# Kernel optimization log

Measured on AMD Instinct MI355X. Metric: run time of the kernel, lower is better.

## Reference

```python
import jax, jax.numpy as jnp
import numpy as np

N_QUBITS = 12
N_LAYERS = 4
BATCH = 1024


def _ry(theta):
    # Batched RY(theta): (...,) -> (..., 2, 2) complex64
    c = jnp.cos(theta / 2)
    s = jnp.sin(theta / 2)
    m = jnp.stack([jnp.stack([c, -s], -1), jnp.stack([s, c], -1)], -2)
    return m.astype(jnp.complex64)


def _rot(phi, theta, omega):
    # PennyLane Rot(phi, theta, omega) = RZ(omega) @ RY(theta) @ RZ(phi)
    c = jnp.cos(theta / 2)
    s = jnp.sin(theta / 2)
    ep = jnp.exp(-0.5j * (phi + omega))  # e^{-i(phi+omega)/2}
    em = jnp.exp(0.5j * (phi - omega))   # e^{ i(phi-omega)/2}
    m00 = ep * c
    m01 = -em * s
    m10 = jnp.conj(em) * s
    m11 = jnp.conj(ep) * c
    m = jnp.stack([jnp.stack([m00, m01], -1), jnp.stack([m10, m11], -1)], -2)
    return m.astype(jnp.complex64)


def _apply_1q(state, U, wire, n):
    # state: (B, 2^n); U: (2,2) or batched (B,2,2). Wire 0 = most significant bit.
    B = state.shape[0]
    st = state.reshape(B, 2 ** wire, 2, 2 ** (n - 1 - wire))
    if U.ndim == 2:
        st = jnp.einsum('ij,bajc->baic', U, st)
    else:
        st = jnp.einsum('bij,bajc->baic', U, st)
    return st.reshape(B, 2 ** n)


def _cnot(state, c, t, n):
    # CNOT(control=c, target=t): flip target bit where control bit == 1.
    B = state.shape[0]
    lo, hi = (c, t) if c < t else (t, c)
    st = state.reshape(B, 2 ** lo, 2, 2 ** (hi - lo - 1), 2, 2 ** (n - 1 - hi))
    c_ax = 2 if c < t else 4
    t_ax = 6 - c_ax
    s0 = jax.lax.index_in_dim(st, 0, c_ax, keepdims=True)
    s1 = jax.lax.index_in_dim(st, 1, c_ax, keepdims=True)
    s1 = jnp.flip(s1, axis=t_ax)
    st = jnp.concatenate([s0, s1], axis=c_ax)
    return st.reshape(B, 2 ** n)


def _circuit(x, weights):
    # AngleEmbedding(rotation='Y') + StronglyEntanglingLayers + per-wire PauliZ expvals
    B, n = x.shape
    state = jnp.zeros((B, 2 ** n), jnp.complex64).at[:, 0].set(1.0)
    for w in range(n):  # angle embedding: RY(x[:, w]) on wire w (batched gate)
        state = _apply_1q(state, _ry(x[:, w]), w, n)
    n_layers = weights.shape[0]
    for l in range(n_layers):
        for w in range(n):
            state = _apply_1q(state, _rot(weights[l, w, 0], weights[l, w, 1], weights[l, w, 2]), w, n)
        r = (l % (n - 1)) + 1  # default StronglyEntanglingLayers range
        for w in range(n):
            state = _cnot(state, w, (w + r) % n, n)
    probs = jnp.real(state * jnp.conj(state))  # (B, 2^n)
    zs = []
    for w in range(n):
        p = probs.reshape(B, 2 ** w, 2, 2 ** (n - 1 - w))
        zs.append((p[:, :, 0, :] - p[:, :, 1, :]).sum((1, 2)))
    return jnp.stack(zs, -1)  # (B, n) PauliZ expectation values


def setup_inputs() -> dict:
    key = jax.random.key(0)
    k1, k2, k3 = jax.random.split(key, 3)
    x = jax.random.uniform(k1, (BATCH, N_QUBITS), jnp.float32, -jnp.pi, jnp.pi)
    weights = jax.random.uniform(k2, (N_LAYERS, N_QUBITS, 3), jnp.float32, 0.0, 2 * jnp.pi)
    head_w = jax.random.normal(k3, (1, N_QUBITS), jnp.float32) * 0.1
    head_b = jnp.zeros((1,), jnp.float32)
    return {"x": x, "weights": weights, "head_w": head_w, "head_b": head_b}


def reference(x, weights, head_w, head_b):
    z = _circuit(x, weights)              # (B, n_qubits), values in [-1, 1]
    y = z @ head_w.T + head_b             # (B, 1)
    return y[:, 0]                        # squeeze(-1)
```

## Files before the change

### kernel.cpp

```cpp
#include <hip/hip_runtime.h>

#define NQ 12
#define NSTATES 4096
#define NLAYERS 4
#define NGATES 48
#define NMERGED 12
#define NGROUPS 9
#define TPB 256

struct Sched { unsigned m[NGATES]; unsigned sel[NGATES]; unsigned zrow[NQ]; };

constexpr Sched make_sched() {
    Sched s{};
    unsigned rows[NQ] = {}, bcols[NQ] = {};
    for (int b = 0; b < NQ; ++b) { rows[b] = 1u << b; bcols[b] = 1u << b; }
    int g = 0;
    for (int w = 0; w < NQ; ++w) { int b = NQ - 1 - w; s.m[g] = bcols[b]; s.sel[g] = rows[b]; ++g; }
    for (int l = 0; l < NLAYERS; ++l) {
        if (l > 0)
            for (int w = 0; w < NQ; ++w) { int b = NQ - 1 - w; s.m[g] = bcols[b]; s.sel[g] = rows[b]; ++g; }
        int r = (l % (NQ - 1)) + 1;
        for (int w = 0; w < NQ; ++w) {
            int c = w, t = (w + r) % NQ;
            int bc = NQ - 1 - c, bt = NQ - 1 - t;
            rows[bt] ^= rows[bc];
            bcols[bc] ^= bcols[bt];
        }
    }
    for (int w = 0; w < NQ; ++w) s.zrow[w] = rows[NQ - 1 - w];
    return s;
}

constexpr unsigned swz(unsigned j) { return j ^ (((j >> 4) ^ (j >> 8)) & 0xFu); }

struct Group {
    unsigned sel[4];
    unsigned swzc[16];
    unsigned cparbits[4];
    int npos[8];
};
struct Plan {
    Group g[NGROUPS];
    unsigned zrow[NQ];
    unsigned zparbits[NQ];
};

constexpr bool inv4(const unsigned m[4], int p0, int p1, int p2, int p3) {
    int pv[4] = {p0, p1, p2, p3};
    unsigned rows[4] = {};
    for (int i = 0; i < 4; ++i) {
        unsigned r = 0;
        for (int k = 0; k < 4; ++k) r |= ((m[i] >> pv[k]) & 1u) << k;
        rows[i] = r;
    }
    unsigned used = 0; int rank = 0;
    for (int c = 0; c < 4; ++c) {
        int pr = -1;
        for (int r = 0; r < 4; ++r)
            if (!((used >> r) & 1u) && ((rows[r] >> c) & 1u)) { pr = r; break; }
        if (pr < 0) continue;
        used |= 1u << pr; ++rank;
        for (int r = 0; r < 4; ++r)
            if (r != pr && ((rows[r] >> c) & 1u)) rows[r] ^= rows[pr];
    }
    return rank == 4;
}

constexpr int popc12(unsigned v) { int c = 0; for (int i = 0; i < 12; ++i) c += (v >> i) & 1; return c; }
constexpr int msb12(unsigned v) { int m = -1; for (int i = 0; i < 12; ++i) if ((v >> i) & 1) m = i; return m; }

constexpr int coverage(const int piv[4]) {
    bool isp[12] = {};
    for (int i = 0; i < 4; ++i) isp[piv[i]] = true;
    bool seen[4] = {}; int cov = 0, cnt = 0;
    for (int p = 0; p < 12 && cnt < 6; ++p)
        if (!isp[p]) { if (!seen[p & 3]) { seen[p & 3] = true; ++cov; } ++cnt; }
    return cov;
}

constexpr Plan make_plan() {
    Sched s = make_sched();
    Plan pl{};
    for (int w = 0; w < NQ; ++w) pl.zrow[w] = s.zrow[w];
    for (int gi = 0; gi < NGROUPS; ++gi) {
        Group &G = pl.g[gi];
        unsigned m[4] = {};
        for (int i = 0; i < 4; ++i) {
            m[i] = s.m[NMERGED + gi * 4 + i];
            G.sel[i] = s.sel[NMERGED + gi * 4 + i];
        }
        int piv[4] = {};
        unsigned bas[4] = {};
        for (int i = 0; i < 4; ++i) {
            unsigned v = m[i];
            for (int k = 0; k < i; ++k) if ((v >> piv[k]) & 1u) v ^= bas[k];
            piv[i] = msb12(v);
            bas[i] = v;
        }
        if (coverage(piv) < 4) {
            int best[4] = {piv[0], piv[1], piv[2], piv[3]};
            int bestcov = coverage(piv);
            for (int a = 0; a < 4 && bestcov < 4; ++a) {
                for (int q = 0; q < 12 && bestcov < 4; ++q) {
                    bool dup = false;
                    for (int i = 0; i < 4; ++i) if (piv[i] == q) dup = true;
                    if (dup) continue;
                    int cand[4] = {piv[0], piv[1], piv[2], piv[3]};
                    cand[a] = q;
                    if (!inv4(m, cand[0], cand[1], cand[2], cand[3])) continue;
                    int cv = coverage(cand);
                    if (cv > bestcov) { bestcov = cv; for (int i = 0; i < 4; ++i) best[i] = cand[i]; }
                }
            }
            for (int i = 0; i < 4; ++i) piv[i] = best[i];
        }
        {
            bool isp[12] = {};
            for (int i = 0; i < 4; ++i) isp[piv[i]] = true;
            int k = 0;
            for (int p = 0; p < 12; ++p) if (!isp[p]) G.npos[k++] = p;
        }
        for (int e = 0; e < 16; ++e) {
            unsigned c = 0;
            for (int q = 0; q < 4; ++q) if ((e >> q) & 1) c ^= m[q];
            G.swzc[e] = swz(c);
        }
        for (int i = 0; i < 4; ++i) {
            unsigned bits = 0;
            for (int e = 0; e < 16; ++e) {
                unsigned c = 0;
                for (int q = 0; q < 4; ++q) if ((e >> q) & 1) c ^= m[q];
                if (popc12(c & G.sel[i]) & 1) bits |= 1u << e;
            }
            G.cparbits[i] = bits;
        }
        if (gi == NGROUPS - 1) {
            for (int w = 0; w < NQ; ++w) {
                unsigned bits = 0;
                for (int e = 0; e < 16; ++e) {
                    unsigned c = 0;
                    for (int q = 0; q < 4; ++q) if ((e >> q) & 1) c ^= m[q];
                    if (popc12(c & s.zrow[w]) & 1) bits |= 1u << e;
                }
                pl.zparbits[w] = bits;
            }
        }
    }
    return pl;
}

__device__ constexpr Plan PLAN = make_plan();

__device__ __forceinline__ float xorf(float a, unsigned s) {
    return __uint_as_float(__float_as_uint(a) ^ s);
}

template <int GI>
__device__ __forceinline__ void do_pass(int tid, float (&ar)[16], float (&ai)[16],
                                        unsigned &jr_out, float2* st, const float4* gmat)
{
    constexpr Group G = PLAN.g[GI];

    unsigned jr = 0;
    #pragma unroll
    for (int k = 0; k < 8; ++k) jr |= ((unsigned)(tid >> k) & 1u) << G.npos[k];
    const unsigned basev = jr ^ (((jr >> 4) ^ (jr >> 8)) & 0xFu);

    #pragma unroll
    for (int e = 0; e < 8; ++e) {
        float2 v = st[basev ^ G.swzc[e]];
        ar[e] = v.x; ai[e] = v.y;
    }

    {
        const float4 uv = gmat[NMERGED + GI * 4 + 0];
        const unsigned sgP = (unsigned)(__popc(jr & G.sel[0]) & 1) << 31;
        const float ur = uv.x, vi = uv.w;
        const float ui_p = xorf(uv.y, sgP), ui_n = xorf(uv.y, sgP ^ 0x80000000u);
        const float vr_p = xorf(uv.z, sgP), vr_n = xorf(uv.z, sgP ^ 0x80000000u);
        #pragma unroll
        for (int e = 0; e < 8; e += 2) {
            const int f = e | 1;
            const bool neg = ((G.cparbits[0] >> e) & 1u) != 0;
            const float ui = neg ? ui_n : ui_p;
            const float vr = neg ? vr_n : vr_p;
            const float xr_ = ar[e], xi_ = ai[e];
            const float yr_ = ar[f], yi_ = ai[f];
            ar[e] = fmaf(ur, xr_, fmaf(-ui, xi_, fmaf(vr, yr_, -vi * yi_)));
            ai[e] = fmaf(ur, xi_, fmaf( ui, xr_, fmaf(vr, yi_,  vi * yr_)));
            ar[f] = fmaf(ur, yr_, fmaf( ui, yi_, fmaf(-vr, xr_, -vi * xi_)));
            ai[f] = fmaf(ur, yi_, fmaf(-ui, yr_, fmaf(-vr, xi_,  vi * xr_)));
        }
        #pragma unroll
        for (int e = 8; e < 16; ++e) {
            float2 v = st[basev ^ G.swzc[e]];
            ar[e] = v.x; ai[e] = v.y;
        }
        #pragma unroll
        for (int e = 8; e < 16; e += 2) {
            const int f = e | 1;
            const bool neg = ((G.cparbits[0] >> e) & 1u) != 0;
            const float ui = neg ? ui_n : ui_p;
            const float vr = neg ? vr_n : vr_p;
            const float xr_ = ar[e], xi_ = ai[e];
            const float yr_ = ar[f], yi_ = ai[f];
            ar[e] = fmaf(ur, xr_, fmaf(-ui, xi_, fmaf(vr, yr_, -vi * yi_)));
            ai[e] = fmaf(ur, xi_, fmaf( ui, xr_, fmaf(vr, yi_,  vi * yr_)));
            ar[f] = fmaf(ur, yr_, fmaf( ui, yi_, fmaf(-vr, xr_, -vi * xi_)));
            ai[f] = fmaf(ur, yi_, fmaf(-ui, yr_, fmaf(-vr, xi_,  vi * xr_)));
        }
    }

    #pragma unroll
    for (int i = 1; i < 4; ++i) {
        const float4 uv = gmat[NMERGED + GI * 4 + i];
        const unsigned sgP = (unsigned)(__popc(jr & G.sel[i]) & 1) << 31;
        const float ur = uv.x, vi = uv.w;
        const float ui_p = xorf(uv.y, sgP), ui_n = xorf(uv.y, sgP ^ 0x80000000u);
        const float vr_p = xorf(uv.z, sgP), vr_n = xorf(uv.z, sgP ^ 0x80000000u);
        #pragma unroll
        for (int e = 0; e < 16; ++e) {
            if (e & (1 << i)) continue;
            const int f = e | (1 << i);
            const bool neg = ((G.cparbits[i] >> e) & 1u) != 0;
            const float ui = neg ? ui_n : ui_p;
            const float vr = neg ? vr_n : vr_p;
            const float xr_ = ar[e], xi_ = ai[e];
            const float yr_ = ar[f], yi_ = ai[f];
            ar[e] = fmaf(ur, xr_, fmaf(-ui, xi_, fmaf(vr, yr_, -vi * yi_)));
            ai[e] = fmaf(ur, xi_, fmaf( ui, xr_, fmaf(vr, yi_,  vi * yr_)));
            ar[f] = fmaf(ur, yr_, fmaf( ui, yi_, fmaf(-vr, xr_, -vi * xi_)));
            ai[f] = fmaf(ur, yi_, fmaf(-ui, yr_, fmaf(-vr, xi_,  vi * xr_)));
        }
    }

    if constexpr (GI < NGROUPS - 1) {
        #pragma unroll
        for (int e = 0; e < 16; ++e)
            st[basev ^ G.swzc[e]] = make_float2(ar[e], ai[e]);
        __syncthreads();
    }
    jr_out = jr;
}

template <int GI>
__device__ __forceinline__ void run_from(int tid, float (&ar)[16], float (&ai)[16],
                                         unsigned &jr, float2* st, const float4* gmat)
{
    do_pass<GI>(tid, ar, ai, jr, st, gmat);
    if constexpr (GI + 1 < NGROUPS) run_from<GI + 1>(tid, ar, ai, jr, st, gmat);
}

__global__ __launch_bounds__(TPB)
__attribute__((amdgpu_waves_per_eu(4, 4)))
void qreg_kernel(
    const float* __restrict__ x,
    const float* __restrict__ W,
    const float* __restrict__ hw,
    const float* __restrict__ hb,
    float* __restrict__ out)
{
    __shared__ float2 st[NSTATES];
    __shared__ float4 gmat[NGATES];
    __shared__ float red[TPB / 64];

    const int tid = threadIdx.x;
    const int b = blockIdx.x;

    if (tid < NGATES) {
        const int l = tid / NQ;
        const int w = tid % NQ;
        const float* wp = W + tid * 3;
        float phi = wp[0], th = wp[1], om = wp[2];
        float sn, cs;  sincosf(0.5f * th, &sn, &cs);
        float sa, ca;  sincosf(0.5f * (phi + om), &sa, &ca);
        float sb, cb;  sincosf(0.5f * (phi - om), &sb, &cb);
        float u2r = ca * cs, u2i = -sa * cs;
        float v2r = -cb * sn, v2i = -sb * sn;
        float ur, ui, vr, vi;
        if (l == 0) {
            float s1, c1; sincosf(0.5f * x[b * NQ + w], &s1, &c1);
            ur = u2r * c1 + v2r * s1;  ui = u2i * c1 + v2i * s1;
            vr = v2r * c1 - u2r * s1;  vi = v2i * c1 - u2i * s1;
        } else {
            ur = u2r; ui = u2i; vr = v2r; vi = v2i;
        }
        gmat[tid] = make_float4(ur, ui, vr, vi);
    }
    __syncthreads();

    float ar[16], ai[16];

    {
        float pr = 1.0f, pi = 0.0f;
        #pragma unroll
        for (int k = 7; k >= 0; --k) {
            const float4 g = gmat[7 - k];
            const bool bset = ((tid >> k) & 1) != 0;
            const float fr = bset ? -g.z : g.x;
            const float fi = bset ?  g.w : g.y;
            const float nr = fmaf(pr, fr, -pi * fi);
            const float ni = fmaf(pr, fi,  pi * fr);
            pr = nr; pi = ni;
        }
        float t2r[2], t2i[2];
        {   const float4 g = gmat[8];
            t2r[0] = fmaf(pr,  g.x, -pi * g.y);  t2i[0] = fmaf(pr, g.y,  pi * g.x);
            t2r[1] = fmaf(pr, -g.z, -pi * g.w);  t2i[1] = fmaf(pr, g.w, -pi * g.z);
        }
        float t4r[4], t4i[4];
        {   const float4 g = gmat[9];
            #pragma unroll
            for (int h = 0; h < 2; ++h) {
                t4r[2*h]   = fmaf(t2r[h],  g.x, -t2i[h] * g.y);
                t4i[2*h]   = fmaf(t2r[h],  g.y,  t2i[h] * g.x);
                t4r[2*h+1] = fmaf(t2r[h], -g.z, -t2i[h] * g.w);
                t4i[2*h+1] = fmaf(t2r[h],  g.w, -t2i[h] * g.z);
            }
        }
        float t8r[8], t8i[8];
        {   const float4 g = gmat[10];
            #pragma unroll
            for (int h = 0; h < 4; ++h) {
                t8r[2*h]   = fmaf(t4r[h],  g.x, -t4i[h] * g.y);
                t8i[2*h]   = fmaf(t4r[h],  g.y,  t4i[h] * g.x);
                t8r[2*h+1] = fmaf(t4r[h], -g.z, -t4i[h] * g.w);
                t8i[2*h+1] = fmaf(t4r[h],  g.w, -t4i[h] * g.z);
            }
        }
        {   const float4 g = gmat[11];
            #pragma unroll
            for (int h = 0; h < 8; ++h) {
                ar[2*h]   = fmaf(t8r[h],  g.x, -t8i[h] * g.y);
                ai[2*h]   = fmaf(t8r[h],  g.y,  t8i[h] * g.x);
                ar[2*h+1] = fmaf(t8r[h], -g.z, -t8i[h] * g.w);
                ai[2*h+1] = fmaf(t8r[h],  g.w, -t8i[h] * g.z);
            }
        }
        const unsigned hh = ((unsigned)tid ^ ((unsigned)tid >> 4)) & 0xFu;
        const unsigned base = (unsigned)tid << 4;
        #pragma unroll
        for (int e = 0; e < 16; ++e)
            st[base | ((unsigned)e ^ hh)] = make_float2(ar[e], ai[e]);
    }
    __syncthreads();

    unsigned jr = 0;
    run_from<0>(tid, ar, ai, jr, st, gmat);

    float hws[NQ];
    #pragma unroll
    for (int w = 0; w < NQ; ++w) {
        const unsigned sg = (unsigned)(__popc(jr & PLAN.zrow[w]) & 1) << 31;
        hws[w] = xorf(hw[w], sg);
    }
    float acc = 0.0f;
    #pragma unroll
    for (int e = 0; e < 16; ++e) {
        const float prob = fmaf(ar[e], ar[e], ai[e] * ai[e]);
        float coef = 0.0f;
        #pragma unroll
        for (int w = 0; w < NQ; ++w)
            coef += ((PLAN.zparbits[w] >> e) & 1u) ? -hws[w] : hws[w];
        acc = fmaf(prob, coef, acc);
    }

    #pragma unroll
    for (int o = 32; o > 0; o >>= 1) acc += __shfl_xor(acc, o, 64);
    if ((tid & 63) == 0) red[tid >> 6] = acc;
    __syncthreads();
    if (tid == 0) out[b] = red[0] + red[1] + red[2] + red[3] + hb[0];
}

extern "C" void kernel_launch(void* const* d_in, const int* in_sizes, int n_in,
                              void* d_out, int out_size, void* d_ws, size_t ws_size,
                              hipStream_t stream) {
    const float* x  = (const float*)d_in[0];
    const float* W  = (const float*)d_in[1];
    const float* hw = (const float*)d_in[2];
    const float* hb = (const float*)d_in[3];
    float* out = (float*)d_out;

    int B = in_sizes[0] / NQ;
    qreg_kernel<<<B, TPB, 0, stream>>>(x, W, hw, hb, out);
}
```

Measured before the change: 88.45 us.

## Regroup gates into triples with 512 threads holding 8 amplitudes each

Each shared-memory pass now fuses 3 gates instead of 4, so there are 12 passes instead of 9. Each thread holds 8 complex amplitudes instead of 16, and the block doubles to 512 threads with the waves-per-EU target raised to 8. The constexpr planning (pivot selection, swizzle offsets, parity masks) and the initial product-state construction are adapted to the 9-bit thread index. The aim is lower register pressure and more latency hiding through higher occupancy. The cost is more LDS round trips and __syncthreads barriers per circuit, and it assumes the reduction buffer holds TPB/64 entries.

```diff
diff --git a/kernel.cpp b/kernel.cpp
--- a/kernel.cpp
+++ b/kernel.cpp
@@ -5,8 +5,8 @@
 #define NLAYERS 4
 #define NGATES 48
 #define NMERGED 12
-#define NGROUPS 9
-#define TPB 256
+#define NGROUPS 12
+#define TPB 512
 
 struct Sched { unsigned m[NGATES]; unsigned sel[NGATES]; unsigned zrow[NQ]; };
 
@@ -34,10 +34,10 @@
 constexpr unsigned swz(unsigned j) { return j ^ (((j >> 4) ^ (j >> 8)) & 0xFu); }
 
 struct Group {
-    unsigned sel[4];
-    unsigned swzc[16];
-    unsigned cparbits[4];
-    int npos[8];
+    unsigned sel[3];
+    unsigned swzc[8];
+    unsigned cparbits[3];
+    int npos[9];
 };
 struct Plan {
     Group g[NGROUPS];
@@ -45,33 +45,33 @@
     unsigned zparbits[NQ];
 };
 
-constexpr bool inv4(const unsigned m[4], int p0, int p1, int p2, int p3) {
-    int pv[4] = {p0, p1, p2, p3};
-    unsigned rows[4] = {};
-    for (int i = 0; i < 4; ++i) {
+constexpr bool inv3(const unsigned m[3], int p0, int p1, int p2) {
+    int pv[3] = {p0, p1, p2};
+    unsigned rows[3] = {};
+    for (int i = 0; i < 3; ++i) {
         unsigned r = 0;
-        for (int k = 0; k < 4; ++k) r |= ((m[i] >> pv[k]) & 1u) << k;
+        for (int k = 0; k < 3; ++k) r |= ((m[i] >> pv[k]) & 1u) << k;
         rows[i] = r;
     }
     unsigned used = 0; int rank = 0;
-    for (int c = 0; c < 4; ++c) {
+    for (int c = 0; c < 3; ++c) {
         int pr = -1;
-        for (int r = 0; r < 4; ++r)
+        for (int r = 0; r < 3; ++r)
             if (!((used >> r) & 1u) && ((rows[r] >> c) & 1u)) { pr = r; break; }
         if (pr < 0) continue;
         used |= 1u << pr; ++rank;
-        for (int r = 0; r < 4; ++r)
+        for (int r = 0; r < 3; ++r)
             if (r != pr && ((rows[r] >> c) & 1u)) rows[r] ^= rows[pr];
     }
-    return rank == 4;
+    return rank == 3;
 }
 
 constexpr int popc12(unsigned v) { int c = 0; for (int i = 0; i < 12; ++i) c += (v >> i) & 1; return c; }
 constexpr int msb12(unsigned v) { int m = -1; for (int i = 0; i < 12; ++i) if ((v >> i) & 1) m = i; return m; }
 
-constexpr int coverage(const int piv[4]) {
+constexpr int coverage3(const int piv[3]) {
     bool isp[12] = {};
-    for (int i = 0; i < 4; ++i) isp[piv[i]] = true;
+    for (int i = 0; i < 3; ++i) isp[piv[i]] = true;
     bool seen[4] = {}; int cov = 0, cnt = 0;
     for (int p = 0; p < 12 && cnt < 6; ++p)
         if (!isp[p]) { if (!seen[p & 3]) { seen[p & 3] = true; ++cov; } ++cnt; }
@@ -84,52 +84,52 @@
     for (int w = 0; w < NQ; ++w) pl.zrow[w] = s.zrow[w];
     for (int gi = 0; gi < NGROUPS; ++gi) {
         Group &G = pl.g[gi];
-        unsigned m[4] = {};
-        for (int i = 0; i < 4; ++i) {
-            m[i] = s.m[NMERGED + gi * 4 + i];
-            G.sel[i] = s.sel[NMERGED + gi * 4 + i];
-        }
-        int piv[4] = {};
-        unsigned bas[4] = {};
-        for (int i = 0; i < 4; ++i) {
+        unsigned m[3] = {};
+        for (int i = 0; i < 3; ++i) {
+            m[i] = s.m[NMERGED + gi * 3 + i];
+            G.sel[i] = s.sel[NMERGED + gi * 3 + i];
+        }
+        int piv[3] = {};
+        unsigned bas[3] = {};
+        for (int i = 0; i < 3; ++i) {
             unsigned v = m[i];
             for (int k = 0; k < i; ++k) if ((v >> piv[k]) & 1u) v ^= bas[k];
             piv[i] = msb12(v);
             bas[i] = v;
         }
-        if (coverage(piv) < 4) {
-            int best[4] = {piv[0], piv[1], piv[2], piv[3]};
-            int bestcov = coverage(piv);
-            for (int a = 0; a < 4 && bestcov < 4; ++a) {
+        if (coverage3(piv) < 4) {
+            int best[3] = {piv[0], piv[1], piv[2]};
+            int bestcov = coverage3(piv);
+            for (int a = 0; a < 3 && bestcov < 4; ++a) {
                 for (int q = 0; q < 12 && bestcov < 4; ++q) {
                     bool dup = false;
-                    for (int i = 0; i < 4; ++i) if (piv[i] == q) dup = true;
+                    for (int i = 0; i < 3; ++i) if (piv[i] == q) dup = true;
                     if (dup) continue;
-                    int cand[4] = {piv[0], piv[1], piv[2], piv[3]};
+                    int cand[3] = {piv[0], piv[1], piv[2]};
                     cand[a] = q;
-                    if (!inv4(m, cand[0], cand[1], cand[2], cand[3])) continue;
-                    int cv = coverage(cand);
-                    if (cv > bestcov) { bestcov = cv; for (int i = 0; i < 4; ++i) best[i] = cand[i]; }
+                    if (!inv3(m, cand[0], cand[1], cand[2])) continue;
+                    int cv = coverage3(cand);
+                    if (cv > bestcov) { bestcov = cv; for (int i = 0; i < 3; ++i) best[i] = cand[i]; }
                 }
             }
-            for (int i = 0; i < 4; ++i) piv[i] = best[i];
+            for (int i = 0; i < 3; ++i) piv[i] = best[i];
         }
         {
             bool isp[12] = {};
-            for (int i = 0; i < 4; ++i) isp[piv[i]] = true;
+            for (int i = 0; i < 3; ++i) isp[piv[i]] = true;
             int k = 0;
             for (int p = 0; p < 12; ++p) if (!isp[p]) G.npos[k++] = p;
         }
-        for (int e = 0; e < 16; ++e) {
+        for (int e = 0; e < 8; ++e) {
             unsigned c = 0;
-            for (int q = 0; q < 4; ++q) if ((e >> q) & 1) c ^= m[q];
+            for (int q = 0; q < 3; ++q) if ((e >> q) & 1) c ^= m[q];
             G.swzc[e] = swz(c);
         }
-        for (int i = 0; i < 4; ++i) {
+        for (int i = 0; i < 3; ++i) {
             unsigned bits = 0;
-            for (int e = 0; e < 16; ++e) {
+            for (int e = 0; e < 8; ++e) {
                 unsigned c = 0;
-                for (int q = 0; q < 4; ++q) if ((e >> q) & 1) c ^= m[q];
+                for (int q = 0; q < 3; ++q) if ((e >> q) & 1) c ^= m[q];
                 if (popc12(c & G.sel[i]) & 1) bits |= 1u << e;
             }
             G.cparbits[i] = bits;
@@ -137,9 +137,9 @@
         if (gi == NGROUPS - 1) {
             for (int w = 0; w < NQ; ++w) {
                 unsigned bits = 0;
-                for (int e = 0; e < 16; ++e) {
+                for (int e = 0; e < 8; ++e) {
                     unsigned c = 0;
-                    for (int q = 0; q < 4; ++q) if ((e >> q) & 1) c ^= m[q];
+                    for (int q = 0; q < 3; ++q) if ((e >> q) & 1) c ^= m[q];
                     if (popc12(c & s.zrow[w]) & 1) bits |= 1u << e;
                 }
                 pl.zparbits[w] = bits;
@@ -155,88 +155,71 @@
     return __uint_as_float(__float_as_uint(a) ^ s);
 }
 
+#define BFLY(ip, e, f)                                                        \
+    {                                                                         \
+        const bool neg = ((G.cparbits[ip] >> (e)) & 1u) != 0;                 \
+        const float ui = neg ? ui_n : ui_p;                                   \
+        const float vr = neg ? vr_n : vr_p;                                   \
+        const float xr_ = ar[e], xi_ = ai[e];                                 \
+        const float yr_ = ar[f], yi_ = ai[f];                                 \
+        ar[e] = fmaf(ur, xr_, fmaf(-ui, xi_, fmaf(vr, yr_, -vi * yi_)));      \
+        ai[e] = fmaf(ur, xi_, fmaf( ui, xr_, fmaf(vr, yi_,  vi * yr_)));      \
+        ar[f] = fmaf(ur, yr_, fmaf( ui, yi_, fmaf(-vr, xr_, -vi * xi_)));     \
+        ai[f] = fmaf(ur, yi_, fmaf(-ui, yr_, fmaf(-vr, xi_,  vi * xr_)));     \
+    }
+
 template <int GI>
-__device__ __forceinline__ void do_pass(int tid, float (&ar)[16], float (&ai)[16],
+__device__ __forceinline__ void do_pass(int tid, float (&ar)[8], float (&ai)[8],
                                         unsigned &jr_out, float2* st, const float4* gmat)
 {
     constexpr Group G = PLAN.g[GI];
 
     unsigned jr = 0;
     #pragma unroll
-    for (int k = 0; k < 8; ++k) jr |= ((unsigned)(tid >> k) & 1u) << G.npos[k];
+    for (int k = 0; k < 9; ++k) jr |= ((unsigned)(tid >> k) & 1u) << G.npos[k];
     const unsigned basev = jr ^ (((jr >> 4) ^ (jr >> 8)) & 0xFu);
 
     #pragma unroll
-    for (int e = 0; e < 8; ++e) {
+    for (int e = 0; e < 4; ++e) {
         float2 v = st[basev ^ G.swzc[e]];
         ar[e] = v.x; ai[e] = v.y;
     }
 
     {
-        const float4 uv = gmat[NMERGED + GI * 4 + 0];
+        const float4 uv = gmat[NMERGED + GI * 3 + 0];
         const unsigned sgP = (unsigned)(__popc(jr & G.sel[0]) & 1) << 31;
         const float ur = uv.x, vi = uv.w;
         const float ui_p = xorf(uv.y, sgP), ui_n = xorf(uv.y, sgP ^ 0x80000000u);
         const float vr_p = xorf(uv.z, sgP), vr_n = xorf(uv.z, sgP ^ 0x80000000u);
-        #pragma unroll
-        for (int e = 0; e < 8; e += 2) {
-            const int f = e | 1;
-            const bool neg = ((G.cparbits[0] >> e) & 1u) != 0;
-            const float ui = neg ? ui_n : ui_p;
-            const float vr = neg ? vr_n : vr_p;
-            const float xr_ = ar[e], xi_ = ai[e];
-            const float yr_ = ar[f], yi_ = ai[f];
-            ar[e] = fmaf(ur, xr_, fmaf(-ui, xi_, fmaf(vr, yr_, -vi * yi_)));
-            ai[e] = fmaf(ur, xi_, fmaf( ui, xr_, fmaf(vr, yi_,  vi * yr_)));
-            ar[f] = fmaf(ur, yr_, fmaf( ui, yi_, fmaf(-vr, xr_, -vi * xi_)));
-            ai[f] = fmaf(ur, yi_, fmaf(-ui, yr_, fmaf(-vr, xi_,  vi * xr_)));
-        }
-        #pragma unroll
-        for (int e = 8; e < 16; ++e) {
+        BFLY(0, 0, 1)
+        BFLY(0, 2, 3)
+        #pragma unroll
+        for (int e = 4; e < 8; ++e) {
             float2 v = st[basev ^ G.swzc[e]];
             ar[e] = v.x; ai[e] = v.y;
         }
-        #pragma unroll
-        for (int e = 8; e < 16; e += 2) {
-            const int f = e | 1;
-            const bool neg = ((G.cparbits[0] >> e) & 1u) != 0;
-            const float ui = neg ? ui_n : ui_p;
-            const float vr = neg ? vr_n : vr_p;
-            const float xr_ = ar[e], xi_ = ai[e];
-            const float yr_ = ar[f], yi_ = ai[f];
-            ar[e] = fmaf(ur, xr_, fmaf(-ui, xi_, fmaf(vr, yr_, -vi * yi_)));
-            ai[e] = fmaf(ur, xi_, fmaf( ui, xr_, fmaf(vr, yi_,  vi * yr_)));
-            ar[f] = fmaf(ur, yr_, fmaf( ui, yi_, fmaf(-vr, xr_, -vi * xi_)));
-            ai[f] = fmaf(ur, yi_, fmaf(-ui, yr_, fmaf(-vr, xi_,  vi * xr_)));
-        }
-    }
-
-    #pragma unroll
-    for (int i = 1; i < 4; ++i) {
-        const float4 uv = gmat[NMERGED + GI * 4 + i];
+        BFLY(0, 4, 5)
+        BFLY(0, 6, 7)
+    }
+
+    #pragma unroll
+    for (int i = 1; i < 3; ++i) {
+        const float4 uv = gmat[NMERGED + GI * 3 + i];
         const unsigned sgP = (unsigned)(__popc(jr & G.sel[i]) & 1) << 31;
         const float ur = uv.x, vi = uv.w;
         const float ui_p = xorf(uv.y, sgP), ui_n = xorf(uv.y, sgP ^ 0x80000000u);
         const float vr_p = xorf(uv.z, sgP), vr_n = xorf(uv.z, sgP ^ 0x80000000u);
         #pragma unroll
-        for (int e = 0; e < 16; ++e) {
+        for (int e = 0; e < 8; ++e) {
             if (e & (1 << i)) continue;
             const int f = e | (1 << i);
-            const bool neg = ((G.cparbits[i] >> e) & 1u) != 0;
-            const float ui = neg ? ui_n : ui_p;
-            const float vr = neg ? vr_n : vr_p;
-            const float xr_ = ar[e], xi_ = ai[e];
-            const float yr_ = ar[f], yi_ = ai[f];
-            ar[e] = fmaf(ur, xr_, fmaf(-ui, xi_, fmaf(vr, yr_, -vi * yi_)));
-            ai[e] = fmaf(ur, xi_, fmaf( ui, xr_, fmaf(vr, yi_,  vi * yr_)));
-            ar[f] = fmaf(ur, yr_, fmaf( ui, yi_, fmaf(-vr, xr_, -vi * xi_)));
-            ai[f] = fmaf(ur, yi_, fmaf(-ui, yr_, fmaf(-vr, xi_,  vi * xr_)));
+            BFLY(i, e, f)
         }
     }
 
     if constexpr (GI < NGROUPS - 1) {
         #pragma unroll
-        for (int e = 0; e < 16; ++e)
+        for (int e = 0; e < 8; ++e)
             st[basev ^ G.swzc[e]] = make_float2(ar[e], ai[e]);
         __syncthreads();
     }
@@ -244,7 +227,7 @@
 }
 
 template <int GI>
-__device__ __forceinline__ void run_from(int tid, float (&ar)[16], float (&ai)[16],
+__device__ __forceinline__ void run_from(int tid, float (&ar)[8], float (&ai)[8],
                                          unsigned &jr, float2* st, const float4* gmat)
 {
     do_pass<GI>(tid, ar, ai, jr, st, gmat);
@@ -252,7 +235,7 @@
 }
 
 __global__ __launch_bounds__(TPB)
-__attribute__((amdgpu_waves_per_eu(4, 4)))
+__attribute__((amdgpu_waves_per_eu(8, 8)))
 void qreg_kernel(
     const float* __restrict__ x,
     const float* __restrict__ W,
@@ -289,13 +272,13 @@
     }
     __syncthreads();
 
-    float ar[16], ai[16];
+    float ar[8], ai[8];
 
     {
         float pr = 1.0f, pi = 0.0f;
         #pragma unroll
-        for (int k = 7; k >= 0; --k) {
-            const float4 g = gmat[7 - k];
+        for (int k = 8; k >= 0; --k) {
+            const float4 g = gmat[8 - k];
             const bool bset = ((tid >> k) & 1) != 0;
             const float fr = bset ? -g.z : g.x;
             const float fi = bset ?  g.w : g.y;
@@ -304,12 +287,12 @@
             pr = nr; pi = ni;
         }
         float t2r[2], t2i[2];
-        {   const float4 g = gmat[8];
+        {   const float4 g = gmat[9];
             t2r[0] = fmaf(pr,  g.x, -pi * g.y);  t2i[0] = fmaf(pr, g.y,  pi * g.x);
             t2r[1] = fmaf(pr, -g.z, -pi * g.w);  t2i[1] = fmaf(pr, g.w, -pi * g.z);
         }
         float t4r[4], t4i[4];
-        {   const float4 g = gmat[9];
+        {   const float4 g = gmat[10];
             #pragma unroll
             for (int h = 0; h < 2; ++h) {
                 t4r[2*h]   = fmaf(t2r[h],  g.x, -t2i[h] * g.y);
@@ -318,30 +301,20 @@
                 t4i[2*h+1] = fmaf(t2r[h],  g.w, -t2i[h] * g.z);
             }
         }
-        float t8r[8], t8i[8];
-        {   const float4 g = gmat[10];
+        {   const float4 g = gmat[11];
             #pragma unroll
             for (int h = 0; h < 4; ++h) {
-                t8r[2*h]   = fmaf(t4r[h],  g.x, -t4i[h] * g.y);
-                t8i[2*h]   = fmaf(t4r[h],  g.y,  t4i[h] * g.x);
-                t8r[2*h+1] = fmaf(t4r[h], -g.z, -t4i[h] * g.w);
-                t8i[2*h+1] = fmaf(t4r[h],  g.w, -t4i[h] * g.z);
-            }
-        }
-        {   const float4 g = gmat[11];
-            #pragma unroll
-            for (int h = 0; h < 8; ++h) {
-                ar[2*h]   = fmaf(t8r[h],  g.x, -t8i[h] * g.y);
-                ai[2*h]   = fmaf(t8r[h],  g.y,  t8i[h] * g.x);
-                ar[2*h+1] = fmaf(t8r[h], -g.z, -t8i[h] * g.w);
-                ai[2*h+1] = fmaf(t8r[h],  g.w, -t8i[h] * g.z);
-            }
-        }
-        const unsigned hh = ((unsigned)tid ^ ((unsigned)tid >> 4)) & 0xFu;
-        const unsigned base = (unsigned)tid << 4;
-        #pragma unroll
-        for (int e = 0; e < 16; ++e)
-            st[base | ((unsigned)e ^ hh)] = make_float2(ar[e], ai[e]);
+                ar[2*h]   = fmaf(t4r[h],  g.x, -t4i[h] * g.y);
+                ai[2*h]   = fmaf(t4r[h],  g.y,  t4i[h] * g.x);
+                ar[2*h+1] = fmaf(t4r[h], -g.z, -t4i[h] * g.w);
+                ai[2*h+1] = fmaf(t4r[h],  g.w, -t4i[h] * g.z);
+            }
+        }
+        const unsigned hh = (((unsigned)tid >> 1) ^ ((unsigned)tid >> 5)) & 0xFu;
+        const unsigned base = (unsigned)tid << 3;
+        #pragma unroll
+        for (int e = 0; e < 8; ++e)
+            st[(base | (unsigned)e) ^ hh] = make_float2(ar[e], ai[e]);
     }
     __syncthreads();
 
@@ -356,7 +329,7 @@
     }
     float acc = 0.0f;
     #pragma unroll
-    for (int e = 0; e < 16; ++e) {
+    for (int e = 0; e < 8; ++e) {
         const float prob = fmaf(ar[e], ar[e], ai[e] * ai[e]);
         float coef = 0.0f;
         #pragma unroll
@@ -369,7 +342,12 @@
     for (int o = 32; o > 0; o >>= 1) acc += __shfl_xor(acc, o, 64);
     if ((tid & 63) == 0) red[tid >> 6] = acc;
     __syncthreads();
-    if (tid == 0) out[b] = red[0] + red[1] + red[2] + red[3] + hb[0];
+    if (tid == 0) {
+        float tot = 0.0f;
+        #pragma unroll
+        for (int i = 0; i < TPB / 64; ++i) tot += red[i];
+        out[b] = tot + hb[0];
+    }
 }
 
 extern "C" void kernel_launch(void* const* d_in, const int* in_sizes, int n_in,
```

Measured after the change: 89.52 us. Within noise of the previous version (+1.2%).
